# Kernel optimization log

Measured on AMD Instinct MI355X. Metric: run time of the kernel, lower is better.

The kernel has to match this reference:

```python
import jax, jax.numpy as jnp
import numpy as np

TEMP = 1.0
POOL_K = 0.5
BN_EPS = 1e-5
B, N, D = 16, 256, 128


def setup_inputs() -> dict:
    key = jax.random.key(0)
    ks = jax.random.split(key, 8)
    s = 0.05
    return {
        "x": jax.random.normal(ks[0], (B, N, D), jnp.float32),
        "att_proj_w": jax.random.normal(ks[1], (D, D), jnp.float32) * s,
        "att_proj_b": jnp.zeros((D,), jnp.float32),
        "att_weight": jax.random.normal(ks[2], (D, 1), jnp.float32) * s,
        "pwa_w": jax.random.normal(ks[3], (D, D), jnp.float32) * s,
        "pwa_b": jnp.zeros((D,), jnp.float32),
        "pwoa_w": jax.random.normal(ks[4], (D, D), jnp.float32) * s,
        "pwoa_b": jnp.zeros((D,), jnp.float32),
        "bn_gamma": jnp.ones((D,), jnp.float32),
        "bn_beta": jnp.zeros((D,), jnp.float32),
        "bn_mean": jnp.zeros((D,), jnp.float32),
        "bn_var": jnp.ones((D,), jnp.float32),
        "pool_w": jax.random.normal(ks[5], (D, 1), jnp.float32) * s,
        "pool_b": jnp.zeros((1,), jnp.float32),
    }


def reference(x, att_proj_w, att_proj_b, att_weight, pwa_w, pwa_b,
              pwoa_w, pwoa_b, bn_gamma, bn_beta, bn_mean, bn_var,
              pool_w, pool_b):
    # ---- GraphAttentionLayer (eval mode: dropout = identity) ----
    # pairwise node outer product: (B, N, N, D)
    pair = x[:, :, None, :] * x[:, None, :, :]
    # att_proj + tanh, then project to scalar per node pair
    a = jnp.tanh(pair @ att_proj_w + att_proj_b)          # (B,N,N,D)
    logits = (a @ att_weight)[..., 0] / TEMP              # (B,N,N)
    # softmax over dim=-2 (the first node axis of the (N,N) map)
    att = jax.nn.softmax(logits, axis=1)                  # (B,N,N)
    # project: att_map @ x through proj_with_att, plus skip branch
    agg = jnp.einsum("bij,bjd->bid", att, x)              # (B,N,D)
    h = (agg @ pwa_w + pwa_b) + (x @ pwoa_w + pwoa_b)
    # BatchNorm1d in eval mode over feature dim
    h = (h - bn_mean) * jax.lax.rsqrt(bn_var + BN_EPS) * bn_gamma + bn_beta
    h = jax.nn.selu(h)
    # ---- GraphPool (eval mode: dropout = identity) ----
    scores = jax.nn.sigmoid(h @ pool_w + pool_b)          # (B,N,1)
    k_nodes = max(int(N * POOL_K), 1)
    _, idx = jax.lax.top_k(scores[..., 0], k_nodes)       # (B,k)
    hs = h * scores                                       # (B,N,D)
    out = jnp.take_along_axis(hs, idx[:, :, None], axis=1)  # (B,k,D)
    return out
```

## Files before the change

### kernel.cpp

```cpp
#include <hip/hip_runtime.h>
#include <math.h>

typedef float f32x4 __attribute__((ext_vector_type(4)));
typedef short s16x8 __attribute__((ext_vector_type(8)));

#define L2E 1.4426950408889634f
#define C2L2E 2.885390081777927f

__global__ void k0_prep(const float* __restrict__ W,
                        unsigned short* __restrict__ gWhi,
                        unsigned short* __restrict__ gWlo,
                        float* __restrict__ S) {
  int bid = blockIdx.x;
  if (bid < 64) {
    int t = bid * 256 + threadIdx.x;
    int d = t >> 7, e = t & 127;
    float w = W[d * 128 + e];
    unsigned u = __float_as_uint(w);
    unsigned hb = (u + 0x7fffu + ((u >> 16) & 1u)) >> 16;
    float r = w - __uint_as_float(hb << 16);
    unsigned ul = __float_as_uint(r);
    unsigned lb = (ul + 0x7fffu + ((ul >> 16) & 1u)) >> 16;
    int addr = e * 128 + (d ^ ((e & 7) << 3));
    gWhi[addr] = (unsigned short)hb;
    gWlo[addr] = (unsigned short)lb;
  } else {
    S[(bid - 64) * 256 + threadIdx.x] = 0.f;
  }
}

__global__ __launch_bounds__(512, 4) void kA_logits(
    const float* __restrict__ x, const unsigned short* __restrict__ gWhi,
    const unsigned short* __restrict__ gWlo, const float* __restrict__ apb,
    const float* __restrict__ av, float* __restrict__ Lg,
    float* __restrict__ S) {
  __shared__ __align__(16) unsigned short sWhi[16384];
  __shared__ __align__(16) unsigned short sWlo[16384];
  __shared__ __align__(16) float sXj[16 * 132];
  __shared__ float sRow[16][8];
  __shared__ float sMir[16];

  int tt = blockIdx.x, ti = 0;
  while (tt >= 16 - ti) { tt -= 16 - ti; ++ti; }
  const int tj = ti + tt;
  const int b = blockIdx.y;
  const int i0 = ti * 16, j0 = tj * 16;
  const int tid = threadIdx.x;

  {
    const uint4* shi = (const uint4*)gWhi;
    const uint4* slo = (const uint4*)gWlo;
    uint4* dhi = (uint4*)sWhi;
    uint4* dlo = (uint4*)sWlo;
#pragma unroll
    for (int r = 0; r < 4; ++r) {
      dhi[tid + 512 * r] = shi[tid + 512 * r];
      dlo[tid + 512 * r] = slo[tid + 512 * r];
    }
    const float4* xsrc = (const float4*)(x + ((size_t)(b * 256 + j0)) * 128);
    *(float4*)&sXj[(tid >> 5) * 132 + (tid & 31) * 4] = xsrc[tid];
  }
  __syncthreads();

  const int lane = tid & 63;
  const int w = tid >> 6;
  const int quad = lane >> 4;
  const int col = lane & 15;
  const int swz = (col & 7) << 3;

  float vw[8];
  f32x4 acc[2][8];
#pragma unroll
  for (int et = 0; et < 8; ++et) {
    float bi = apb[col + 16 * et];
    vw[et] = av[col + 16 * et];
#pragma unroll
    for (int mt = 0; mt < 2; ++mt) acc[mt][et] = (f32x4){bi, bi, bi, bi};
  }

  const float* xib = x + ((size_t)(b * 256 + i0 + 2 * w)) * 128;

#pragma unroll
  for (int kstep = 0; kstep < 4; ++kstep) {
    const int k0 = kstep * 32 + quad * 8;
    float4 xj0 = *(const float4*)&sXj[col * 132 + k0];
    float4 xj1 = *(const float4*)&sXj[col * 132 + k0 + 4];
    s16x8 Ah[2], Al[2];
#pragma unroll
    for (int mt = 0; mt < 2; ++mt) {
      const float* xip = xib + mt * 128 + k0;
      float4 xi0 = *(const float4*)xip;
      float4 xi1 = *(const float4*)(xip + 4);
      float pv[8];
      pv[0] = xi0.x * xj0.x; pv[1] = xi0.y * xj0.y;
      pv[2] = xi0.z * xj0.z; pv[3] = xi0.w * xj0.w;
      pv[4] = xi1.x * xj1.x; pv[5] = xi1.y * xj1.y;
      pv[6] = xi1.z * xj1.z; pv[7] = xi1.w * xj1.w;
      uint4 hp, lp;
      unsigned* hq = (unsigned*)&hp;
      unsigned* lq = (unsigned*)&lp;
#pragma unroll
      for (int p = 0; p < 4; ++p) {
        unsigned u0 = __float_as_uint(pv[2 * p]);
        unsigned u1 = __float_as_uint(pv[2 * p + 1]);
        hq[p] = __builtin_amdgcn_perm(u1, u0, 0x07060302);
        float h0 = __uint_as_float(u0 & 0xffff0000u);
        float h1 = __uint_as_float(u1 & 0xffff0000u);
        unsigned v0 = __float_as_uint(pv[2 * p] - h0) + 0x8000u;
        unsigned v1 = __float_as_uint(pv[2 * p + 1] - h1) + 0x8000u;
        lq[p] = __builtin_amdgcn_perm(v1, v0, 0x07060302);
      }
      Ah[mt] = *(s16x8*)&hp;
      Al[mt] = *(s16x8*)&lp;
    }
#pragma unroll
    for (int et = 0; et < 8; ++et) {
      const int addr = (col + 16 * et) * 128 + (k0 ^ swz);
      s16x8 bh = *(const s16x8*)&sWhi[addr];
      s16x8 bl = *(const s16x8*)&sWlo[addr];
#pragma unroll
      for (int mt = 0; mt < 2; ++mt) {
        acc[mt][et] = __builtin_amdgcn_mfma_f32_16x16x32_bf16(Ah[mt], bh, acc[mt][et], 0, 0, 0);
        acc[mt][et] = __builtin_amdgcn_mfma_f32_16x16x32_bf16(Al[mt], bh, acc[mt][et], 0, 0, 0);
        acc[mt][et] = __builtin_amdgcn_mfma_f32_16x16x32_bf16(Ah[mt], bl, acc[mt][et], 0, 0, 0);
      }
    }
  }

  float E[2];
#pragma unroll
  for (int mt = 0; mt < 2; ++mt) {
    float ls[4] = {0.f, 0.f, 0.f, 0.f};
#pragma unroll
    for (int et = 0; et < 8; ++et) {
#pragma unroll
      for (int r = 0; r < 4; ++r) {
        float e2 = __builtin_amdgcn_exp2f(acc[mt][et][r] * C2L2E);
        float t = 1.0f - 2.0f * __builtin_amdgcn_rcpf(e2 + 1.0f);
        ls[r] += t * vw[et];
      }
    }
#pragma unroll
    for (int m = 1; m < 16; m <<= 1) {
      ls[0] += __shfl_xor(ls[0], m);
      ls[1] += __shfl_xor(ls[1], m);
      ls[2] += __shfl_xor(ls[2], m);
      ls[3] += __shfl_xor(ls[3], m);
    }
    float fl = (col == 0) ? ls[0] : (col == 1) ? ls[1] : (col == 2) ? ls[2] : ls[3];
    E[mt] = __builtin_amdgcn_exp2f(fl * L2E);
  }

  if (col < 4) {
    const int j = j0 + quad * 4 + col;
    float2 val = {E[0], E[1]};
    *(float2*)&Lg[((size_t)(b * 256 + j)) * 256 + i0 + 2 * w] = val;
    sRow[quad * 4 + col][w] = E[0] + E[1];
  }

  if (ti != tj) {
    if (col < 4) {
      const int j = j0 + quad * 4 + col;
#pragma unroll
      for (int mt = 0; mt < 2; ++mt)
        Lg[((size_t)(b * 256 + i0 + 2 * w + mt)) * 256 + j] = E[mt];
    }
#pragma unroll
    for (int mt = 0; mt < 2; ++mt) {
      float v = (col < 4) ? E[mt] : 0.f;
#pragma unroll
      for (int m = 1; m < 64; m <<= 1) v += __shfl_xor(v, m);
      if (lane == 0) sMir[2 * w + mt] = v;
    }
  }
  __syncthreads();
  if (tid < 16) {
    float rs = sRow[tid][0];
#pragma unroll
    for (int q = 1; q < 8; ++q) rs += sRow[tid][q];
    atomicAdd(&S[b * 256 + j0 + tid], rs);
    if (ti != tj) atomicAdd(&S[b * 256 + i0 + tid], sMir[tid]);
  }
}

__global__ __launch_bounds__(256) void kB_aggh(
    const float* __restrict__ Lg, const float* __restrict__ S,
    const float* __restrict__ x,
    const float* __restrict__ pwa, const float* __restrict__ pwoa,
    const float* __restrict__ pwab, const float* __restrict__ pwob,
    const float* __restrict__ gam, const float* __restrict__ bet,
    const float* __restrict__ mea, const float* __restrict__ varr,
    const float* __restrict__ plw, const float* __restrict__ plb,
    float* __restrict__ h, float* __restrict__ scores) {
  const int b = blockIdx.y, i0 = blockIdx.x * 8;
  const int tid = threadIdx.x;
  const int il = tid >> 5, dl = tid & 31;
  __shared__ float sInv[256];
  __shared__ float satt[8][256];
  __shared__ __align__(16) float sxj[2][32 * 128];
  __shared__ float sa[1024];
  __shared__ float sxi[1024];
  __shared__ double sScD[8][32];

  const float4* xb = (const float4*)(x + ((size_t)b * 256) * 128);

  sInv[tid] = 1.0f / S[b * 256 + tid];
  ((float4*)sxi)[tid] = ((const float4*)(x + ((size_t)(b * 256 + i0)) * 128))[tid];
  const float4* lsrc = (const float4*)(Lg + ((size_t)(b * 256 + i0)) * 256);
  float4 l0 = lsrc[tid];
  float4 l1 = lsrc[tid + 256];
#pragma unroll
  for (int r = 0; r < 4; ++r)
    ((float4*)sxj[0])[tid + 256 * r] = xb[tid + 256 * r];
  __syncthreads();
  {
    const int j0q = (tid * 4) & 255;
    float s0 = sInv[j0q], s1 = sInv[j0q + 1], s2 = sInv[j0q + 2], s3 = sInv[j0q + 3];
    l0.x *= s0; l0.y *= s1; l0.z *= s2; l0.w *= s3;
    l1.x *= s0; l1.y *= s1; l1.z *= s2; l1.w *= s3;
    ((float4*)satt)[tid] = l0;
    ((float4*)satt)[tid + 256] = l1;
  }
  __syncthreads();

  float acc[4] = {0.f, 0.f, 0.f, 0.f};
  for (int c = 0; c < 8; ++c) {
    const int cb = c & 1;
    float4 p0, p1, p2, p3;
    if (c < 7) {
      const float4* src = xb + (c + 1) * 1024;
      p0 = src[tid]; p1 = src[tid + 256]; p2 = src[tid + 512]; p3 = src[tid + 768];
    }
#pragma unroll
    for (int jl = 0; jl < 32; ++jl) {
      float a = satt[il][c * 32 + jl];
      float4 xv = *(const float4*)&sxj[cb][jl * 128 + dl * 4];
      acc[0] += a * xv.x; acc[1] += a * xv.y;
      acc[2] += a * xv.z; acc[3] += a * xv.w;
    }
    if (c < 7) {
      float4* dst = (float4*)sxj[cb ^ 1];
      dst[tid] = p0; dst[tid + 256] = p1; dst[tid + 512] = p2; dst[tid + 768] = p3;
      __syncthreads();
    }
  }

  *(float4*)&sa[il * 128 + dl * 4] = *(float4*)acc;
  __syncthreads();

  double z[4] = {0, 0, 0, 0};
#pragma unroll 8
  for (int k = 0; k < 128; ++k) {
    double a = (double)sa[il * 128 + k];
    float4 wv = *(const float4*)(pwa + k * 128 + dl * 4);
    z[0] += a * (double)wv.x; z[1] += a * (double)wv.y;
    z[2] += a * (double)wv.z; z[3] += a * (double)wv.w;
  }
#pragma unroll 8
  for (int k = 0; k < 128; ++k) {
    double a = (double)sxi[il * 128 + k];
    float4 wv = *(const float4*)(pwoa + k * 128 + dl * 4);
    z[0] += a * (double)wv.x; z[1] += a * (double)wv.y;
    z[2] += a * (double)wv.z; z[3] += a * (double)wv.w;
  }
  float o[4];
#pragma unroll
  for (int q = 0; q < 4; ++q) {
    int d = dl * 4 + q;
    double hv = z[q] + (double)pwab[d] + (double)pwob[d];
    double bn = (hv - (double)mea[d]) * (1.0 / sqrt((double)varr[d] + 1e-5)) *
                    (double)gam[d] +
                (double)bet[d];
    float bf = (float)bn;
    o[q] = bf > 0.f ? 1.0507009873554805f * bf
                    : 1.7580993408473766f *
                          (__builtin_amdgcn_exp2f(bf * L2E) - 1.0f);
  }
  *(float4*)(h + ((size_t)(b * 256 + i0 + il)) * 128 + dl * 4) = *(float4*)o;

  sScD[il][dl] = (double)o[0] * (double)plw[dl * 4] +
                 (double)o[1] * (double)plw[dl * 4 + 1] +
                 (double)o[2] * (double)plw[dl * 4 + 2] +
                 (double)o[3] * (double)plw[dl * 4 + 3];
  __syncthreads();
  if (tid < 8) {
    double zz = (double)plb[0];
    for (int c = 0; c < 32; ++c) zz += sScD[tid][c];
    scores[b * 256 + i0 + tid] = (float)(1.0 / (1.0 + exp(-zz)));
  }
}

__global__ __launch_bounds__(1024) void kC_topk(const float* __restrict__ h,
                                                const float* __restrict__ scores,
                                                float* __restrict__ out) {
  const int bq = blockIdx.x;
  const int b = bq >> 2, qp = bq & 3;
  const int tid = threadIdx.x;
  const int t = tid >> 2, c = tid & 3;
  __shared__ float sc[256];
  __shared__ int ipart[256][4];
  __shared__ int sel[128];

  if (c == 0) sc[t] = scores[b * 256 + t];
  __syncthreads();
  {
    const float st = sc[t];
    int r = 0;
    for (int m = c * 64; m < c * 64 + 64; ++m) {
      float sm = sc[m];
      r += (sm > st) || (sm == st && m < t);
    }
    ipart[t][c] = r;
  }
  __syncthreads();
  if (c == 0) {
    int rank = ipart[t][0] + ipart[t][1] + ipart[t][2] + ipart[t][3];
    if (rank < 128) sel[rank] = t;
  }
  __syncthreads();
  const float4* h4 = (const float4*)(h + (size_t)b * 256 * 128);
  float4* o4 = (float4*)(out + (size_t)b * 128 * 128);
  const int row = qp * 32 + (tid >> 5);
  const int q = tid & 31;
  int src = sel[row];
  float ss = sc[src];
  float4 hv = h4[src * 32 + q];
  float4 ov;
  ov.x = hv.x * ss; ov.y = hv.y * ss; ov.z = hv.z * ss; ov.w = hv.w * ss;
  o4[row * 32 + q] = ov;
}

extern "C" void kernel_launch(void* const* d_in, const int* in_sizes, int n_in,
                              void* d_out, int out_size, void* d_ws, size_t ws_size,
                              hipStream_t stream) {
  const float* x    = (const float*)d_in[0];
  const float* apw  = (const float*)d_in[1];
  const float* apb  = (const float*)d_in[2];
  const float* av   = (const float*)d_in[3];
  const float* pwa  = (const float*)d_in[4];
  const float* pwab = (const float*)d_in[5];
  const float* pwoa = (const float*)d_in[6];
  const float* pwob = (const float*)d_in[7];
  const float* gam  = (const float*)d_in[8];
  const float* bet  = (const float*)d_in[9];
  const float* mea  = (const float*)d_in[10];
  const float* varr = (const float*)d_in[11];
  const float* plw  = (const float*)d_in[12];
  const float* plb  = (const float*)d_in[13];
  float* out = (float*)d_out;

  unsigned short* gWhi = (unsigned short*)d_ws;
  unsigned short* gWlo = gWhi + 16384;
  float* S  = (float*)((char*)d_ws + 65536);
  float* Lg = (float*)((char*)d_ws + 81920);
  float* hb = Lg + (size_t)16 * 256 * 256;
  float* sco = hb + (size_t)16 * 256 * 128;

  k0_prep<<<80, 256, 0, stream>>>(apw, gWhi, gWlo, S);
  kA_logits<<<dim3(136, 16), 512, 0, stream>>>(x, gWhi, gWlo, apb, av, Lg, S);
  kB_aggh<<<dim3(32, 16), 256, 0, stream>>>(Lg, S, x, pwa, pwoa, pwab, pwob,
                                            gam, bet, mea, varr, plw, plb, hb, sco);
  kC_topk<<<64, 1024, 0, stream>>>(hb, sco, out);
}
```

Before: 168.0 us.

## Fuse top-k pooling into aggregation kernel via last-block-per-batch counter

Removes the separate top-k kernel launch. Each aggregation block bumps a per-batch atomic counter after writing its scores, and the last of the 32 blocks for that batch ranks all 256 scores and gathers the top 128 scaled rows into the output. This saves one kernel launch and its dependency gap. In exchange, the whole gather for a batch runs on a single 256-thread block with serialized 256-step rank loops, and correctness depends on the threadfence/atomic protocol.

New measurement: 208.6 us. 24.1% more time.

```diff
diff --git a/kernel.cpp b/kernel.cpp
--- a/kernel.cpp
+++ b/kernel.cpp
@@ -10,7 +10,7 @@
 __global__ void k0_prep(const float* __restrict__ W,
                         unsigned short* __restrict__ gWhi,
                         unsigned short* __restrict__ gWlo,
-                        float* __restrict__ S) {
+                        float* __restrict__ S, int* __restrict__ cnt) {
   int bid = blockIdx.x;
   if (bid < 64) {
     int t = bid * 256 + threadIdx.x;
@@ -26,6 +26,7 @@
     gWlo[addr] = (unsigned short)lb;
   } else {
     S[(bid - 64) * 256 + threadIdx.x] = 0.f;
+    if (bid == 64 && threadIdx.x < 16) cnt[threadIdx.x] = 0;
   }
 }
 
@@ -191,7 +192,8 @@
     const float* __restrict__ gam, const float* __restrict__ bet,
     const float* __restrict__ mea, const float* __restrict__ varr,
     const float* __restrict__ plw, const float* __restrict__ plb,
-    float* __restrict__ h, float* __restrict__ scores) {
+    float* __restrict__ h, float* __restrict__ scores,
+    int* __restrict__ cnt, float* __restrict__ out) {
   const int b = blockIdx.y, i0 = blockIdx.x * 8;
   const int tid = threadIdx.x;
   const int il = tid >> 5, dl = tid & 31;
@@ -201,6 +203,7 @@
   __shared__ float sa[1024];
   __shared__ float sxi[1024];
   __shared__ double sScD[8][32];
+  __shared__ int sLast;
 
   const float4* xb = (const float4*)(x + ((size_t)b * 256) * 128);
 
@@ -288,46 +291,44 @@
     for (int c = 0; c < 32; ++c) zz += sScD[tid][c];
     scores[b * 256 + i0 + tid] = (float)(1.0 / (1.0 + exp(-zz)));
   }
-}
-
-__global__ __launch_bounds__(1024) void kC_topk(const float* __restrict__ h,
-                                                const float* __restrict__ scores,
-                                                float* __restrict__ out) {
-  const int bq = blockIdx.x;
-  const int b = bq >> 2, qp = bq & 3;
-  const int tid = threadIdx.x;
-  const int t = tid >> 2, c = tid & 3;
-  __shared__ float sc[256];
-  __shared__ int ipart[256][4];
-  __shared__ int sel[128];
-
-  if (c == 0) sc[t] = scores[b * 256 + t];
+
+  __threadfence();
+  __syncthreads();
+  if (tid == 0) sLast = atomicAdd(&cnt[b], 1);
+  __syncthreads();
+  if (sLast != 31) return;
+  __threadfence();
+
+  float* sc = sxj[0];
+  int* sel = (int*)(sxj[0] + 256);
+
+  sc[tid] = scores[b * 256 + tid];
   __syncthreads();
   {
-    const float st = sc[t];
+    const float st = sc[tid];
     int r = 0;
-    for (int m = c * 64; m < c * 64 + 64; ++m) {
+    for (int m = 0; m < 256; ++m) {
       float sm = sc[m];
-      r += (sm > st) || (sm == st && m < t);
-    }
-    ipart[t][c] = r;
-  }
-  __syncthreads();
-  if (c == 0) {
-    int rank = ipart[t][0] + ipart[t][1] + ipart[t][2] + ipart[t][3];
-    if (rank < 128) sel[rank] = t;
-  }
-  __syncthreads();
-  const float4* h4 = (const float4*)(h + (size_t)b * 256 * 128);
-  float4* o4 = (float4*)(out + (size_t)b * 128 * 128);
-  const int row = qp * 32 + (tid >> 5);
-  const int q = tid & 31;
-  int src = sel[row];
-  float ss = sc[src];
-  float4 hv = h4[src * 32 + q];
-  float4 ov;
-  ov.x = hv.x * ss; ov.y = hv.y * ss; ov.z = hv.z * ss; ov.w = hv.w * ss;
-  o4[row * 32 + q] = ov;
+      r += (sm > st) || (sm == st && m < tid);
+    }
+    if (r < 128) sel[r] = tid;
+  }
+  __syncthreads();
+  {
+    const float4* h4 = (const float4*)(h + (size_t)b * 256 * 128);
+    float4* o4 = (float4*)(out + (size_t)b * 128 * 128);
+#pragma unroll
+    for (int g = 0; g < 16; ++g) {
+      int v = tid + 256 * g;
+      int row = v >> 5, q = v & 31;
+      int src = sel[row];
+      float ss = sc[src];
+      float4 hv = h4[src * 32 + q];
+      float4 ov;
+      ov.x = hv.x * ss; ov.y = hv.y * ss; ov.z = hv.z * ss; ov.w = hv.w * ss;
+      o4[row * 32 + q] = ov;
+    }
+  }
 }
 
 extern "C" void kernel_launch(void* const* d_in, const int* in_sizes, int n_in,
@@ -355,10 +356,11 @@
   float* Lg = (float*)((char*)d_ws + 81920);
   float* hb = Lg + (size_t)16 * 256 * 256;
   float* sco = hb + (size_t)16 * 256 * 128;
-
-  k0_prep<<<80, 256, 0, stream>>>(apw, gWhi, gWlo, S);
+  int* cnt = (int*)(sco + 16 * 256);
+
+  k0_prep<<<80, 256, 0, stream>>>(apw, gWhi, gWlo, S, cnt);
   kA_logits<<<dim3(136, 16), 512, 0, stream>>>(x, gWhi, gWlo, apb, av, Lg, S);
   kB_aggh<<<dim3(32, 16), 256, 0, stream>>>(Lg, S, x, pwa, pwoa, pwab, pwob,
-                                            gam, bet, mea, varr, plw, plb, hb, sco);
-  kC_topk<<<64, 1024, 0, stream>>>(hb, sco, out);
+                                            gam, bet, mea, varr, plw, plb,
+                                            hb, sco, cnt, out);
 }
```
